# Kernel optimization log

Hardware: AMD Instinct MI355X
Metric: run time of the kernel (lower is better)

The kernel has to match this reference:

```python
import jax, jax.numpy as jnp
import numpy as np
import math

B, S, D = 16, 577, 768          # batch, seq (24*24 grid + 1 cls), in_dim=att_dim
H, HD = 12, 64                  # heads, head_dim
GRID = 24                       # height = width; S = GRID*GRID + rpe_skip
RATIO = 1.9
ALPHA, BETA, GAMMA = 1.0 * RATIO, 2.0 * RATIO, 8.0 * RATIO
BETA_INT = int(BETA)            # 3
NUM_BUCKETS = (2 * BETA_INT + 1) ** 2 + 1  # 49 product buckets + 1 extra for skip (cls) = 50


def _piecewise_index(d):
    # iRPE piecewise bucket index (numpy, static). d: integer offsets.
    d = d.astype(np.float64)
    ad = np.abs(d)
    log_part = ALPHA + np.log(np.maximum(ad, 1e-9) / ALPHA) / math.log(GAMMA / ALPHA) * (BETA - ALPHA)
    y_out = np.sign(d) * np.clip(np.round(log_part), None, BETA)
    idx = np.where(ad <= ALPHA, np.round(d), y_out)
    return np.trunc(idx).astype(np.int64)  # torch .to(int) truncates toward zero


def make_rp_bucket():
    # 2D 'product' method bucket ids with skip=1 (cls token -> extra bucket)
    ii, jj = np.meshgrid(np.arange(GRID), np.arange(GRID), indexing='ij')
    pos = np.stack([ii.ravel(), jj.ravel()], axis=-1)          # (L,2)
    diff = pos[:, None, :] - pos[None, :, :]                    # (L,L,2)
    Sb = 2 * BETA_INT + 1
    r = _piecewise_index(diff[..., 0]) + BETA_INT               # [0, 2*beta_int]
    c = _piecewise_index(diff[..., 1]) + BETA_INT
    pid = r * Sb + c                                            # [0, 48]
    L = GRID * GRID
    bucket = np.full((L + 1, L + 1), NUM_BUCKETS - 1, dtype=np.int32)
    bucket[1:, 1:] = pid
    return jnp.asarray(bucket)


def setup_inputs() -> dict:
    key = jax.random.key(0)
    k1, k2, k3 = jax.random.split(key, 3)
    x = jax.random.normal(k1, (B, S, D), dtype=jnp.float32)
    w_qkv = jax.random.normal(k2, (3 * D, D), dtype=jnp.float32) * 0.02   # torch Linear weight (out,in)
    rpe_table = jax.random.normal(k3, (HD, NUM_BUCKETS), dtype=jnp.float32) * 0.02  # shared-head contextual table
    rp_bucket = make_rp_bucket()                                # (S,S) int32
    return {"x": x, "w_qkv": w_qkv, "rpe_table": rpe_table, "rp_bucket": rp_bucket}


def reference(x, w_qkv, rpe_table, rp_bucket):
    qkv = x @ w_qkv.T                                           # (B,S,3D)
    q, k, v = jnp.split(qkv, 3, axis=-1)
    # Faithful to torch source: plain reshape (B,S,D)->(B,H,S,HD) (no transpose-split)
    scale = 1.0 / jnp.sqrt(jnp.asarray(HD, x.dtype))
    q = q.reshape(B, H, S, HD) * scale
    k = k.reshape(B, H, S, HD)
    v = v.reshape(B, H, S, HD)
    qk = jnp.einsum('bhid,bhjd->bhij', q, k)                    # (B,H,S,S)
    # contextual rpe_k: bias[b,h,i,j] = (q[b,h,i] . rpe_table[:, rp_bucket[i,j]])
    ctx = jnp.einsum('bhid,dc->bhic', q, rpe_table)             # (B,H,S,NUM_BUCKETS)
    idx = jnp.broadcast_to(rp_bucket[None, None].astype(jnp.int32), (B, H, S, S))
    bias = jnp.take_along_axis(ctx, idx, axis=-1)               # (B,H,S,S)
    att = jax.nn.softmax(qk + bias, axis=-1)
    out = jnp.einsum('bhij,bhjd->bhid', att, v)                 # (B,H,S,HD)
    y = out.transpose(0, 2, 1, 3).reshape(B, S, D)              # out_proj is Identity (out_dim==att_dim)
    return y
```

## Files before the change

### kernel.cpp

```cpp
#include <hip/hip_runtime.h>

constexpr int BN_  = 16;
constexpr int SN_  = 577;
constexpr int SP_  = 640;
constexpr int DN_  = 768;
constexpr int HN_  = 12;
constexpr int HD_  = 64;
constexpr int NB_  = 50;
constexpr int MR_  = BN_ * SN_;
constexpr int MRP_ = 73 * 128;
constexpr int NQ_  = 3 * DN_;
constexpr int BHS_ = BN_ * HN_ * SN_;
constexpr int SHD_ = SN_ * HD_;

typedef __attribute__((ext_vector_type(8))) short short8;
typedef __attribute__((ext_vector_type(4))) float f32x4;

__device__ __forceinline__ short f2bf(float f) {
  union { float f; unsigned u; } v; v.f = f;
  unsigned r = (v.u + 0x7fffu + ((v.u >> 16) & 1u)) >> 16;
  return (short)r;
}

__device__ __forceinline__ float ex2(float x) {
  float r; asm("v_exp_f32 %0, %1" : "=v"(r) : "v"(x)); return r;
}

__device__ __forceinline__ unsigned cvtpk(float a, float b) {
  unsigned r; asm("v_cvt_pk_bf16_f32 %0, %1, %2" : "=v"(r) : "v"(a), "v"(b));
  return r;
}

__device__ __forceinline__ float bf2f(unsigned short u) {
  union { unsigned u; float f; } v; v.u = ((unsigned)u) << 16; return v.f;
}

__device__ __forceinline__ void gload16(const void* g, void* l) {
  __builtin_amdgcn_global_load_lds(
      (const __attribute__((address_space(1))) unsigned int*)g,
      (__attribute__((address_space(3))) unsigned int*)l, 16, 0, 0);
}

__launch_bounds__(256)
__global__ void cvt_k(const float* __restrict__ src, short* __restrict__ dst,
                      int n_src, int n_dst) {
  const int i = (blockIdx.x * 256 + threadIdx.x) * 8;
  if (i >= n_dst) return;
  union { short8 v; short u[8]; } pk;
  if (i < n_src) {
    const float4 a = *(const float4*)(src + i);
    const float4 b = *(const float4*)(src + i + 4);
    pk.u[0] = f2bf(a.x); pk.u[1] = f2bf(a.y); pk.u[2] = f2bf(a.z); pk.u[3] = f2bf(a.w);
    pk.u[4] = f2bf(b.x); pk.u[5] = f2bf(b.y); pk.u[6] = f2bf(b.z); pk.u[7] = f2bf(b.w);
  } else {
#pragma unroll
    for (int j = 0; j < 8; ++j) pk.u[j] = 0;
  }
  *(short8*)(dst + i) = pk.v;
}

__launch_bounds__(256)
__global__ void rpb8_k(const int* __restrict__ rpb, unsigned char* __restrict__ rpbu8) {
  const int tid = blockIdx.x * 256 + threadIdx.x;
  if (tid >= SN_ * 160) return;
  const int i = tid / 160, c4 = tid - i * 160;
  const int j = c4 * 4;
  uchar4 o;
  o.x = (j     < SN_) ? (unsigned char)rpb[i * SN_ + j    ] : 0;
  o.y = (j + 1 < SN_) ? (unsigned char)rpb[i * SN_ + j + 1] : 0;
  o.z = (j + 2 < SN_) ? (unsigned char)rpb[i * SN_ + j + 2] : 0;
  o.w = (j + 3 < SN_) ? (unsigned char)rpb[i * SN_ + j + 3] : 0;
  *(uchar4*)(rpbu8 + (size_t)i * 640 + j) = o;
}

__launch_bounds__(256)
__global__ void qkv_mfma_k(const short* __restrict__ xb, const short* __restrict__ wb,
                           short* __restrict__ Qbf, short* __restrict__ Ksw,
                           short* __restrict__ Vbf) {
  __shared__ short SB[32768];
  const int t = threadIdx.x;
  const int w = t >> 6, lane = t & 63, g = lane >> 4, ln = lane & 15;
  const int wm = w >> 1, wn = w & 1;
  const int m0 = blockIdx.y * 128, n0 = blockIdx.x * 128;

  const int rlo = lane >> 3;
  const int gu  = (lane & 7) ^ rlo;
  const short* ga[4]; const short* gb[4];
  int lOff[4];
#pragma unroll
  for (int q = 0; q < 4; ++q) {
    const int rl = w * 32 + q * 8 + rlo;
    ga[q] = xb + (size_t)(m0 + rl) * DN_ + gu * 8;
    gb[q] = wb + (size_t)(n0 + rl) * DN_ + gu * 8;
    lOff[q] = w * 2048 + q * 512;
  }

  f32x4 acc[4][4];
#pragma unroll
  for (int mt = 0; mt < 4; ++mt)
#pragma unroll
    for (int nt = 0; nt < 4; ++nt) acc[mt][nt] = (f32x4){0.f, 0.f, 0.f, 0.f};

#pragma unroll
  for (int q = 0; q < 4; ++q) {
    gload16(ga[q], SB + lOff[q]);
    gload16(gb[q], SB + 16384 + lOff[q]);
  }
  __syncthreads();

  int cur = 0;
  for (int k0 = 0; k0 < DN_; k0 += 64) {
    if (k0 + 64 < DN_) {
      const int nb = (cur ^ 1) * 8192;
#pragma unroll
      for (int q = 0; q < 4; ++q) {
        gload16(ga[q] + k0 + 64, SB + nb + lOff[q]);
        gload16(gb[q] + k0 + 64, SB + 16384 + nb + lOff[q]);
      }
    }
    const short* Ac = SB + cur * 8192;
    const short* Bc = SB + 16384 + cur * 8192;
#pragma unroll
    for (int kc = 0; kc < 2; ++kc) {
      short8 af[4], bf[4];
#pragma unroll
      for (int mt = 0; mt < 4; ++mt) {
        const int row = wm * 64 + mt * 16 + ln;
        const int u = (kc * 4 + g) ^ (row & 7);
        af[mt] = *(const short8*)&Ac[row * 64 + u * 8];
      }
#pragma unroll
      for (int nt = 0; nt < 4; ++nt) {
        const int row = wn * 64 + nt * 16 + ln;
        const int u = (kc * 4 + g) ^ (row & 7);
        bf[nt] = *(const short8*)&Bc[row * 64 + u * 8];
      }
#pragma unroll
      for (int mt = 0; mt < 4; ++mt)
#pragma unroll
        for (int nt = 0; nt < 4; ++nt)
          acc[mt][nt] = __builtin_amdgcn_mfma_f32_16x16x32_bf16(af[mt], bf[nt], acc[mt][nt], 0, 0, 0);
    }
    __syncthreads();
    cur ^= 1;
  }

  const int wbase = w * 4608;
  const int nw0  = n0 + wn * 64;
  const int secg = nw0 / DN_;
  const int cbw  = nw0 - secg * DN_;
  const float QSC = 0.18033688011112042f;
#pragma unroll
  for (int mt = 0; mt < 4; ++mt)
#pragma unroll
    for (int nt = 0; nt < 4; ++nt)
#pragma unroll
      for (int r = 0; r < 4; ++r) {
        float v = acc[mt][nt][r];
        if (secg == 0) v *= QSC;
        SB[wbase + (mt * 16 + 4 * g + r) * 72 + nt * 16 + ln] = f2bf(v);
      }
  const int gm = m0 + wm * 64 + lane;
  if (gm < MR_) {
    const int bb = gm / SN_;
    const int ss = gm - bb * SN_;
    const int pr = ss * DN_ + cbw;
    const int hh = pr / SHD_;
    const int ii = (pr - hh * SHD_) >> 6;
    const size_t ro = (size_t)(bb * HN_ + hh);
    const short* src = SB + wbase + lane * 72;
    if (secg == 0) {
      short* dst = Qbf + (ro * SN_ + ii) * 64;
#pragma unroll
      for (int u = 0; u < 8; ++u)
        *(short8*)(dst + u * 8) = *(const short8*)(src + u * 8);
    } else if (secg == 1) {
      short* dst = Ksw + (ro * SP_ + ii) * 64;
      const int sw = ii & 7;
#pragma unroll
      for (int u = 0; u < 8; ++u)
        *(short8*)(dst + (u ^ sw) * 8) = *(const short8*)(src + u * 8);
    } else {
      short* dst = Vbf + (ro * SP_ + ii) * 64;
#pragma unroll
      for (int u = 0; u < 8; ++u)
        *(short8*)(dst + u * 8) = *(const short8*)(src + u * 8);
    }
  }
}

__launch_bounds__(256)
__global__ void vtr_k(const short* __restrict__ Vbf, short* __restrict__ Vtsw) {
  __shared__ short T[64][72];
  const int t = threadIdx.x;
  const int jt = blockIdx.x, bh = blockIdx.y;
  const int j0 = jt * 64;
  {
    const int r = t >> 2, c0 = (t & 3) * 16;
    const short* src = Vbf + ((size_t)bh * SP_ + j0 + r) * 64 + c0;
    *(short8*)&T[r][c0]     = *(const short8*)(src);
    *(short8*)&T[r][c0 + 8] = *(const short8*)(src + 8);
  }
  __syncthreads();
  const int d = t >> 2;
  short* dst = Vtsw + ((size_t)bh * 64 + d) * SP_;
  const int sw = (d & 7) << 3;
#pragma unroll
  for (int e = 0; e < 4; ++e) {
    const int jl = (t & 3) * 16 + e * 4;
    const int jg = j0 + jl;
    short4 v;
    v.x = (jg + 0 < SN_) ? T[jl + 0][d] : (short)0;
    v.y = (jg + 1 < SN_) ? T[jl + 1][d] : (short)0;
    v.z = (jg + 2 < SN_) ? T[jl + 2][d] : (short)0;
    v.w = (jg + 3 < SN_) ? T[jl + 3][d] : (short)0;
    const int oq = (jg >> 2) & 7;
    const int pq = ((oq & 3) << 1) | (oq >> 2);
    const int p  = (jg & ~31) | (pq << 2);
    *(short4*)&dst[p ^ sw] = v;
  }
}

__launch_bounds__(256)
__global__ void attn_k(const short* __restrict__ Qbf, const short* __restrict__ Ksw,
                       const short* __restrict__ Vtsw, const float* __restrict__ rpe,
                       const unsigned char* __restrict__ rpbu8, float* __restrict__ y) {
  __shared__ short Kt[4096];
  __shared__ short Vt[4096];
  __shared__ unsigned char rpbt[128 * 68];
  __shared__ unsigned short ctxs[4][32][53];
  short (*Rp)[64] = (short (*)[64])rpbt;

  const int t = threadIdx.x;
  const int w = t >> 6, lane = t & 63, g = lane >> 4, ln = lane & 15;
  const int wg = blockIdx.x;
  const int xcd = wg & 7, idx = wg >> 3;
  const int qt = idx % 5;
  const int bh = (idx / 5) * 8 + xcd;
  const int b = bh / HN_, h = bh - b * HN_;
  const int i0 = qt * 128;
  const size_t rb = (size_t)bh * SN_;
  const short* Kbh = Ksw + (size_t)bh * SP_ * 64;
  const short* Vbh = Vtsw + (size_t)bh * 64 * SP_;

  const int tK = t * 8;
  const int vRow = t >> 3, vCol = (t & 7) * 8;
  const int rpRow = t >> 1, rpCol = (t & 1) * 32;
  const int irow_s = (i0 + rpRow <= SN_ - 1) ? (i0 + rpRow) : (SN_ - 1);

  short8 kr0, kr1, vr0, vr1; int4 rp0_, rp1_;
  kr0 = *(const short8*)(Kbh + tK);
  kr1 = *(const short8*)(Kbh + 2048 + tK);
  vr0 = *(const short8*)(Vbh + (size_t)vRow * SP_ + vCol);
  vr1 = *(const short8*)(Vbh + (size_t)(32 + vRow) * SP_ + vCol);
  rp0_ = *(const int4*)(rpbu8 + (size_t)irow_s * 640 + rpCol);
  rp1_ = *(const int4*)(rpbu8 + (size_t)irow_s * 640 + rpCol + 16);

  for (int e = t; e < 64 * 64; e += 256) {
    const int c = e >> 6, d = e & 63;
    Rp[c][d] = (c < NB_) ? f2bf(rpe[d * NB_ + c]) : (short)0;
  }

  short8 qf[2][2];
#pragma unroll
  for (int s = 0; s < 2; ++s) {
    int row = i0 + 32 * w + 16 * s + ln; if (row > SN_ - 1) row = SN_ - 1;
    const short* qp = Qbf + (rb + row) * 64;
    qf[s][0] = *(const short8*)(qp + 8 * g);
    qf[s][1] = *(const short8*)(qp + 32 + 8 * g);
  }

  __syncthreads();

  {
    f32x4 accC[2][4];
#pragma unroll
    for (int s = 0; s < 2; ++s)
#pragma unroll
      for (int ct = 0; ct < 4; ++ct) accC[s][ct] = (f32x4){0.f, 0.f, 0.f, 0.f};
#pragma unroll
    for (int kc = 0; kc < 2; ++kc) {
#pragma unroll
      for (int ct = 0; ct < 4; ++ct) {
        const short8 rf = *(const short8*)&Rp[ct * 16 + ln][kc * 32 + 8 * g];
        accC[0][ct] = __builtin_amdgcn_mfma_f32_16x16x32_bf16(qf[0][kc], rf, accC[0][ct], 0, 0, 0);
        accC[1][ct] = __builtin_amdgcn_mfma_f32_16x16x32_bf16(qf[1][kc], rf, accC[1][ct], 0, 0, 0);
      }
    }
#pragma unroll
    for (int s = 0; s < 2; ++s)
#pragma unroll
      for (int ct = 0; ct < 4; ++ct) {
        const int c = ct * 16 + ln;
        if (c < 53) {
#pragma unroll
          for (int r = 0; r < 4; ++r)
            ctxs[w][16 * s + 4 * g + r][c] = (unsigned short)f2bf(accC[s][ct][r]);
        }
      }
  }

  float m0s = -3e38f, m1s = -3e38f, l0s = 0.f, l1s = 0.f;
  f32x4 accO[2][4];
#pragma unroll
  for (int s = 0; s < 2; ++s)
#pragma unroll
    for (int dt = 0; dt < 4; ++dt) accO[s][dt] = (f32x4){0.f, 0.f, 0.f, 0.f};

  const int swv = (ln & 7) << 3;

  for (int jt = 0; jt < 10; ++jt) {
    __syncthreads();
    *(short8*)&Kt[tK]        = kr0;
    *(short8*)&Kt[2048 + tK] = kr1;
    *(short8*)&Vt[tK]        = vr0;
    *(short8*)&Vt[2048 + tK] = vr1;
    *(int4*)&rpbt[rpRow * 68 + rpCol]      = rp0_;
    *(int4*)&rpbt[rpRow * 68 + rpCol + 16] = rp1_;
    __syncthreads();

    if (jt < 9) {
      const int jn = jt * 64 + 64;
      kr0 = *(const short8*)(Kbh + (size_t)jn * 64 + tK);
      kr1 = *(const short8*)(Kbh + (size_t)jn * 64 + 2048 + tK);
      vr0 = *(const short8*)(Vbh + (size_t)vRow * SP_ + jn + vCol);
      vr1 = *(const short8*)(Vbh + (size_t)(32 + vRow) * SP_ + jn + vCol);
      rp0_ = *(const int4*)(rpbu8 + (size_t)irow_s * 640 + jn + rpCol);
      rp1_ = *(const int4*)(rpbu8 + (size_t)irow_s * 640 + jn + rpCol + 16);
    }

    f32x4 accS[2][4];
#pragma unroll
    for (int s = 0; s < 2; ++s)
#pragma unroll
      for (int nt = 0; nt < 4; ++nt) accS[s][nt] = (f32x4){0.f, 0.f, 0.f, 0.f};
    __builtin_amdgcn_s_setprio(1);
#pragma unroll
    for (int kc = 0; kc < 2; ++kc) {
      const int cb = (kc * 32 + 8 * g) ^ swv;
#pragma unroll
      for (int nt = 0; nt < 4; ++nt) {
        const short8 kf = *(const short8*)&Kt[(nt * 16 + ln) * 64 + cb];
        accS[0][nt] = __builtin_amdgcn_mfma_f32_16x16x32_bf16(kf, qf[0][kc], accS[0][nt], 0, 0, 0);
        accS[1][nt] = __builtin_amdgcn_mfma_f32_16x16x32_bf16(kf, qf[1][kc], accS[1][nt], 0, 0, 0);
      }
    }
    __builtin_amdgcn_s_setprio(0);

    short8 pf[2][2];
#pragma unroll
    for (int s = 0; s < 2; ++s) {
      const unsigned short* cbase = &ctxs[w][16 * s + ln][0];
      const int rpoff = (32 * w + 16 * s + ln) * 68;
      float pv[4][4];
#pragma unroll
      for (int nt = 0; nt < 4; ++nt) {
        const uchar4 bk = *(const uchar4*)&rpbt[rpoff + nt * 16 + 4 * g];
        pv[nt][0] = accS[s][nt][0] + bf2f(cbase[bk.x]);
        pv[nt][1] = accS[s][nt][1] + bf2f(cbase[bk.y]);
        pv[nt][2] = accS[s][nt][2] + bf2f(cbase[bk.z]);
        pv[nt][3] = accS[s][nt][3] + bf2f(cbase[bk.w]);
      }
      if (jt == 9) {
#pragma unroll
        for (int nt = 0; nt < 4; ++nt) {
          const int jb = jt * 64 + nt * 16 + 4 * g;
#pragma unroll
          for (int r = 0; r < 4; ++r)
            if (jb + r >= SN_) pv[nt][r] = -3e38f;
        }
      }

      float& m = (s == 0) ? m0s : m1s;
      float& l = (s == 0) ? l0s : l1s;

      float mq[4];
#pragma unroll
      for (int nt = 0; nt < 4; ++nt)
        mq[nt] = fmaxf(fmaxf(pv[nt][0], pv[nt][1]), fmaxf(pv[nt][2], pv[nt][3]));
      float mx = fmaxf(fmaxf(mq[0], mq[1]), fmaxf(mq[2], mq[3]));
      mx = fmaxf(mx, __shfl_xor(mx, 16));
      mx = fmaxf(mx, __shfl_xor(mx, 32));

      if (__any(mx > m + 8.f)) {
        const float mnew = fmaxf(m, mx);
        const float sc = ex2(m - mnew);
        float scr[4];
#pragma unroll
        for (int r = 0; r < 4; ++r) scr[r] = __shfl(sc, 4 * g + r);
#pragma unroll
        for (int dt = 0; dt < 4; ++dt)
#pragma unroll
          for (int r = 0; r < 4; ++r) accO[s][dt][r] *= scr[r];
        l *= sc;
        m = mnew;
      }

#pragma unroll
      for (int nt = 0; nt < 4; ++nt)
#pragma unroll
        for (int r = 0; r < 4; ++r)
          pv[nt][r] = ex2(pv[nt][r] - m);
      float sq[4];
#pragma unroll
      for (int nt = 0; nt < 4; ++nt)
        sq[nt] = (pv[nt][0] + pv[nt][1]) + (pv[nt][2] + pv[nt][3]);
      float sum = (sq[0] + sq[1]) + (sq[2] + sq[3]);
      sum += __shfl_xor(sum, 16);
      sum += __shfl_xor(sum, 32);
      l += sum;

#pragma unroll
      for (int kc = 0; kc < 2; ++kc) {
        union { short8 v; unsigned wd[4]; } pk;
        pk.wd[0] = cvtpk(pv[2 * kc][0],     pv[2 * kc][1]);
        pk.wd[1] = cvtpk(pv[2 * kc][2],     pv[2 * kc][3]);
        pk.wd[2] = cvtpk(pv[2 * kc + 1][0], pv[2 * kc + 1][1]);
        pk.wd[3] = cvtpk(pv[2 * kc + 1][2], pv[2 * kc + 1][3]);
        pf[s][kc] = pk.v;
      }
    }

    __builtin_amdgcn_s_setprio(1);
#pragma unroll
    for (int kc = 0; kc < 2; ++kc) {
      const int cb = (kc * 32 + 8 * g) ^ swv;
#pragma unroll
      for (int dt = 0; dt < 4; ++dt) {
        const short8 vf = *(const short8*)&Vt[(dt * 16 + ln) * 64 + cb];
        accO[0][dt] = __builtin_amdgcn_mfma_f32_16x16x32_bf16(pf[0][kc], vf, accO[0][dt], 0, 0, 0);
        accO[1][dt] = __builtin_amdgcn_mfma_f32_16x16x32_bf16(pf[1][kc], vf, accO[1][dt], 0, 0, 0);
      }
    }
    __builtin_amdgcn_s_setprio(0);
  }

#pragma unroll
  for (int s = 0; s < 2; ++s) {
    const float lv = (s == 0) ? l0s : l1s;
    float linv[4];
#pragma unroll
    for (int r = 0; r < 4; ++r) linv[r] = 1.f / __shfl(lv, 4 * g + r);
#pragma unroll
    for (int r = 0; r < 4; ++r) {
      const int i = i0 + 32 * w + 16 * s + 4 * g + r;
      if (i >= SN_) continue;
      float* yp = y + ((size_t)b * SN_ + i) * DN_ + h * HD_ + ln;
#pragma unroll
      for (int dt = 0; dt < 4; ++dt) yp[dt * 16] = accO[s][dt][r] * linv[r];
    }
  }
}

extern "C" void kernel_launch(void* const* d_in, const int* in_sizes, int n_in,
                              void* d_out, int out_size, void* d_ws, size_t ws_size,
                              hipStream_t stream) {
  const float* x   = (const float*)d_in[0];
  const float* w   = (const float*)d_in[1];
  const float* rpe = (const float*)d_in[2];
  const int*   rpb = (const int*)d_in[3];
  float* y = (float*)d_out;

  short* xb   = (short*)d_ws;
  short* wb   = xb + (size_t)MRP_ * DN_;
  short* Qbf  = wb + (size_t)NQ_ * DN_;
  short* Ksw  = Qbf + (size_t)BHS_ * HD_;
  short* Vbf  = Ksw + (size_t)BN_ * HN_ * SP_ * 64;
  short* Vtsw = Vbf + (size_t)BN_ * HN_ * SP_ * 64;
  unsigned char* rpbu8 = (unsigned char*)(Vtsw + (size_t)BN_ * HN_ * 64 * SP_);

  cvt_k<<<dim3(MRP_ * DN_ / 2048), 256, 0, stream>>>(x, xb, MR_ * DN_, MRP_ * DN_);
  cvt_k<<<dim3(NQ_ * DN_ / 2048), 256, 0, stream>>>(w, wb, NQ_ * DN_, NQ_ * DN_);
  rpb8_k<<<dim3((SN_ * 160 + 255) / 256), 256, 0, stream>>>(rpb, rpbu8);
  qkv_mfma_k<<<dim3(18, 73), 256, 0, stream>>>(xb, wb, Qbf, Ksw, Vbf);
  vtr_k<<<dim3(10, BN_ * HN_), 256, 0, stream>>>(Vbf, Vtsw);
  attn_k<<<dim3(960), 256, 0, stream>>>(Qbf, Ksw, Vtsw, rpe, rpbu8, y);
}
```

Measured before the change: 143.9 us.

## Merge prep kernels and load bucket ids directly from global in attention

Combines the two fp32-to-bf16 conversion launches and the bucket-to-uint8 launch into a single prep kernel, removing two kernel launches. In the attention kernel, the LDS staging tile for relative-position bucket ids is removed. Each lane now reads its own 4-byte bucket words straight from global (L2-resident) memory every tile, and the rpe table staging reuses the ctx buffer, guarded by an added barrier. This shrinks LDS use, which may raise occupancy, at the cost of per-tile global loads that are issued right before use and so are not prefetched.

```diff
diff --git a/kernel.cpp b/kernel.cpp
--- a/kernel.cpp
+++ b/kernel.cpp
@@ -13,6 +13,10 @@
 constexpr int BHS_ = BN_ * HN_ * SN_;
 constexpr int SHD_ = SN_ * HD_;
 
+constexpr int NBX_ = MRP_ * DN_ / 2048;
+constexpr int NBW_ = NQ_ * DN_ / 2048;
+constexpr int NBR_ = (SN_ * 160 + 255) / 256;
+
 typedef __attribute__((ext_vector_type(8))) short short8;
 typedef __attribute__((ext_vector_type(4))) float f32x4;
 
@@ -42,35 +46,38 @@
 }
 
 __launch_bounds__(256)
-__global__ void cvt_k(const float* __restrict__ src, short* __restrict__ dst,
-                      int n_src, int n_dst) {
-  const int i = (blockIdx.x * 256 + threadIdx.x) * 8;
-  if (i >= n_dst) return;
-  union { short8 v; short u[8]; } pk;
-  if (i < n_src) {
-    const float4 a = *(const float4*)(src + i);
-    const float4 b = *(const float4*)(src + i + 4);
-    pk.u[0] = f2bf(a.x); pk.u[1] = f2bf(a.y); pk.u[2] = f2bf(a.z); pk.u[3] = f2bf(a.w);
-    pk.u[4] = f2bf(b.x); pk.u[5] = f2bf(b.y); pk.u[6] = f2bf(b.z); pk.u[7] = f2bf(b.w);
+__global__ void prep_k(const float* __restrict__ x, short* __restrict__ xb,
+                       const float* __restrict__ w, short* __restrict__ wb,
+                       const int* __restrict__ rpb, unsigned char* __restrict__ rpbu8) {
+  const int bid = blockIdx.x;
+  const int t = threadIdx.x;
+  if (bid < NBX_ + NBW_) {
+    const float* src; short* dst; int n_src, i;
+    if (bid < NBX_) { src = x; dst = xb; n_src = MR_ * DN_; i = (bid * 256 + t) * 8; }
+    else { src = w; dst = wb; n_src = NQ_ * DN_; i = ((bid - NBX_) * 256 + t) * 8; }
+    union { short8 v; short u[8]; } pk;
+    if (i < n_src) {
+      const float4 a = *(const float4*)(src + i);
+      const float4 b = *(const float4*)(src + i + 4);
+      pk.u[0] = f2bf(a.x); pk.u[1] = f2bf(a.y); pk.u[2] = f2bf(a.z); pk.u[3] = f2bf(a.w);
+      pk.u[4] = f2bf(b.x); pk.u[5] = f2bf(b.y); pk.u[6] = f2bf(b.z); pk.u[7] = f2bf(b.w);
+    } else {
+#pragma unroll
+      for (int j = 0; j < 8; ++j) pk.u[j] = 0;
+    }
+    *(short8*)(dst + i) = pk.v;
   } else {
-#pragma unroll
-    for (int j = 0; j < 8; ++j) pk.u[j] = 0;
-  }
-  *(short8*)(dst + i) = pk.v;
-}
-
-__launch_bounds__(256)
-__global__ void rpb8_k(const int* __restrict__ rpb, unsigned char* __restrict__ rpbu8) {
-  const int tid = blockIdx.x * 256 + threadIdx.x;
-  if (tid >= SN_ * 160) return;
-  const int i = tid / 160, c4 = tid - i * 160;
-  const int j = c4 * 4;
-  uchar4 o;
-  o.x = (j     < SN_) ? (unsigned char)rpb[i * SN_ + j    ] : 0;
-  o.y = (j + 1 < SN_) ? (unsigned char)rpb[i * SN_ + j + 1] : 0;
-  o.z = (j + 2 < SN_) ? (unsigned char)rpb[i * SN_ + j + 2] : 0;
-  o.w = (j + 3 < SN_) ? (unsigned char)rpb[i * SN_ + j + 3] : 0;
-  *(uchar4*)(rpbu8 + (size_t)i * 640 + j) = o;
+    const int tid = (bid - NBX_ - NBW_) * 256 + t;
+    if (tid >= SN_ * 160) return;
+    const int i = tid / 160, c4 = tid - i * 160;
+    const int j = c4 * 4;
+    uchar4 o;
+    o.x = (j     < SN_) ? (unsigned char)rpb[i * SN_ + j    ] : 0;
+    o.y = (j + 1 < SN_) ? (unsigned char)rpb[i * SN_ + j + 1] : 0;
+    o.z = (j + 2 < SN_) ? (unsigned char)rpb[i * SN_ + j + 2] : 0;
+    o.w = (j + 3 < SN_) ? (unsigned char)rpb[i * SN_ + j + 3] : 0;
+    *(uchar4*)(rpbu8 + (size_t)i * 640 + j) = o;
+  }
 }
 
 __launch_bounds__(256)
@@ -227,9 +234,8 @@
                        const unsigned char* __restrict__ rpbu8, float* __restrict__ y) {
   __shared__ short Kt[4096];
   __shared__ short Vt[4096];
-  __shared__ unsigned char rpbt[128 * 68];
   __shared__ unsigned short ctxs[4][32][53];
-  short (*Rp)[64] = (short (*)[64])rpbt;
+  short (*Rp)[64] = (short (*)[64])ctxs;
 
   const int t = threadIdx.x;
   const int w = t >> 6, lane = t & 63, g = lane >> 4, ln = lane & 15;
@@ -245,16 +251,17 @@
 
   const int tK = t * 8;
   const int vRow = t >> 3, vCol = (t & 7) * 8;
-  const int rpRow = t >> 1, rpCol = (t & 1) * 32;
-  const int irow_s = (i0 + rpRow <= SN_ - 1) ? (i0 + rpRow) : (SN_ - 1);
-
-  short8 kr0, kr1, vr0, vr1; int4 rp0_, rp1_;
+
+  const int row0 = (i0 + 32 * w + ln      <= SN_ - 1) ? (i0 + 32 * w + ln)      : (SN_ - 1);
+  const int row1 = (i0 + 32 * w + 16 + ln <= SN_ - 1) ? (i0 + 32 * w + 16 + ln) : (SN_ - 1);
+  const unsigned char* rpL[2] = { rpbu8 + (size_t)row0 * 640 + 4 * g,
+                                  rpbu8 + (size_t)row1 * 640 + 4 * g };
+
+  short8 kr0, kr1, vr0, vr1;
   kr0 = *(const short8*)(Kbh + tK);
   kr1 = *(const short8*)(Kbh + 2048 + tK);
   vr0 = *(const short8*)(Vbh + (size_t)vRow * SP_ + vCol);
   vr1 = *(const short8*)(Vbh + (size_t)(32 + vRow) * SP_ + vCol);
-  rp0_ = *(const int4*)(rpbu8 + (size_t)irow_s * 640 + rpCol);
-  rp1_ = *(const int4*)(rpbu8 + (size_t)irow_s * 640 + rpCol + 16);
 
   for (int e = t; e < 64 * 64; e += 256) {
     const int c = e >> 6, d = e & 63;
@@ -272,33 +279,33 @@
 
   __syncthreads();
 
-  {
-    f32x4 accC[2][4];
-#pragma unroll
-    for (int s = 0; s < 2; ++s)
-#pragma unroll
-      for (int ct = 0; ct < 4; ++ct) accC[s][ct] = (f32x4){0.f, 0.f, 0.f, 0.f};
-#pragma unroll
-    for (int kc = 0; kc < 2; ++kc) {
-#pragma unroll
-      for (int ct = 0; ct < 4; ++ct) {
-        const short8 rf = *(const short8*)&Rp[ct * 16 + ln][kc * 32 + 8 * g];
-        accC[0][ct] = __builtin_amdgcn_mfma_f32_16x16x32_bf16(qf[0][kc], rf, accC[0][ct], 0, 0, 0);
-        accC[1][ct] = __builtin_amdgcn_mfma_f32_16x16x32_bf16(qf[1][kc], rf, accC[1][ct], 0, 0, 0);
-      }
-    }
-#pragma unroll
-    for (int s = 0; s < 2; ++s)
-#pragma unroll
-      for (int ct = 0; ct < 4; ++ct) {
-        const int c = ct * 16 + ln;
-        if (c < 53) {
-#pragma unroll
-          for (int r = 0; r < 4; ++r)
-            ctxs[w][16 * s + 4 * g + r][c] = (unsigned short)f2bf(accC[s][ct][r]);
-        }
-      }
-  }
+  f32x4 accC[2][4];
+#pragma unroll
+  for (int s = 0; s < 2; ++s)
+#pragma unroll
+    for (int ct = 0; ct < 4; ++ct) accC[s][ct] = (f32x4){0.f, 0.f, 0.f, 0.f};
+#pragma unroll
+  for (int kc = 0; kc < 2; ++kc) {
+#pragma unroll
+    for (int ct = 0; ct < 4; ++ct) {
+      const short8 rf = *(const short8*)&Rp[ct * 16 + ln][kc * 32 + 8 * g];
+      accC[0][ct] = __builtin_amdgcn_mfma_f32_16x16x32_bf16(qf[0][kc], rf, accC[0][ct], 0, 0, 0);
+      accC[1][ct] = __builtin_amdgcn_mfma_f32_16x16x32_bf16(qf[1][kc], rf, accC[1][ct], 0, 0, 0);
+    }
+  }
+  __syncthreads();
+
+#pragma unroll
+  for (int s = 0; s < 2; ++s)
+#pragma unroll
+    for (int ct = 0; ct < 4; ++ct) {
+      const int c = ct * 16 + ln;
+      if (c < 53) {
+#pragma unroll
+        for (int r = 0; r < 4; ++r)
+          ctxs[w][16 * s + 4 * g + r][c] = (unsigned short)f2bf(accC[s][ct][r]);
+      }
+    }
 
   float m0s = -3e38f, m1s = -3e38f, l0s = 0.f, l1s = 0.f;
   f32x4 accO[2][4];
@@ -315,9 +322,14 @@
     *(short8*)&Kt[2048 + tK] = kr1;
     *(short8*)&Vt[tK]        = vr0;
     *(short8*)&Vt[2048 + tK] = vr1;
-    *(int4*)&rpbt[rpRow * 68 + rpCol]      = rp0_;
-    *(int4*)&rpbt[rpRow * 68 + rpCol + 16] = rp1_;
     __syncthreads();
+
+    unsigned rpg[2][4];
+#pragma unroll
+    for (int s = 0; s < 2; ++s)
+#pragma unroll
+      for (int nt = 0; nt < 4; ++nt)
+        rpg[s][nt] = *(const unsigned*)(rpL[s] + jt * 64 + nt * 16);
 
     if (jt < 9) {
       const int jn = jt * 64 + 64;
@@ -325,8 +337,6 @@
       kr1 = *(const short8*)(Kbh + (size_t)jn * 64 + 2048 + tK);
       vr0 = *(const short8*)(Vbh + (size_t)vRow * SP_ + jn + vCol);
       vr1 = *(const short8*)(Vbh + (size_t)(32 + vRow) * SP_ + jn + vCol);
-      rp0_ = *(const int4*)(rpbu8 + (size_t)irow_s * 640 + jn + rpCol);
-      rp1_ = *(const int4*)(rpbu8 + (size_t)irow_s * 640 + jn + rpCol + 16);
     }
 
     f32x4 accS[2][4];
@@ -351,15 +361,14 @@
 #pragma unroll
     for (int s = 0; s < 2; ++s) {
       const unsigned short* cbase = &ctxs[w][16 * s + ln][0];
-      const int rpoff = (32 * w + 16 * s + ln) * 68;
       float pv[4][4];
 #pragma unroll
       for (int nt = 0; nt < 4; ++nt) {
-        const uchar4 bk = *(const uchar4*)&rpbt[rpoff + nt * 16 + 4 * g];
-        pv[nt][0] = accS[s][nt][0] + bf2f(cbase[bk.x]);
-        pv[nt][1] = accS[s][nt][1] + bf2f(cbase[bk.y]);
-        pv[nt][2] = accS[s][nt][2] + bf2f(cbase[bk.z]);
-        pv[nt][3] = accS[s][nt][3] + bf2f(cbase[bk.w]);
+        union { unsigned u; uchar4 c; } bk; bk.u = rpg[s][nt];
+        pv[nt][0] = accS[s][nt][0] + bf2f(cbase[bk.c.x]);
+        pv[nt][1] = accS[s][nt][1] + bf2f(cbase[bk.c.y]);
+        pv[nt][2] = accS[s][nt][2] + bf2f(cbase[bk.c.z]);
+        pv[nt][3] = accS[s][nt][3] + bf2f(cbase[bk.c.w]);
       }
       if (jt == 9) {
 #pragma unroll
@@ -469,9 +478,7 @@
   short* Vtsw = Vbf + (size_t)BN_ * HN_ * SP_ * 64;
   unsigned char* rpbu8 = (unsigned char*)(Vtsw + (size_t)BN_ * HN_ * 64 * SP_);
 
-  cvt_k<<<dim3(MRP_ * DN_ / 2048), 256, 0, stream>>>(x, xb, MR_ * DN_, MRP_ * DN_);
-  cvt_k<<<dim3(NQ_ * DN_ / 2048), 256, 0, stream>>>(w, wb, NQ_ * DN_, NQ_ * DN_);
-  rpb8_k<<<dim3((SN_ * 160 + 255) / 256), 256, 0, stream>>>(rpb, rpbu8);
+  prep_k<<<dim3(NBX_ + NBW_ + NBR_), 256, 0, stream>>>(x, xb, w, wb, rpb, rpbu8);
   qkv_mfma_k<<<dim3(18, 73), 256, 0, stream>>>(xb, wb, Qbf, Ksw, Vbf);
   vtr_k<<<dim3(10, BN_ * HN_), 256, 0, stream>>>(Vbf, Vtsw);
   attn_k<<<dim3(960), 256, 0, stream>>>(Qbf, Ksw, Vtsw, rpe, rpbu8, y);
```

After: 152.0 us. 1.06x slower.
